# Kernel tuning notes

Measured on AMD Instinct MI355X. Metric: run time of the kernel, lower is better.

## Reference

```python
import jax, jax.numpy as jnp
import numpy as np

D = 256   # state.D, per-node vector width
B = 16    # batch
L = 8     # depth layers (hidden), all < t_budget
N = 128   # nodes per depth layer
LAMBDA_ASYNC = 0.08
LAMBDA_TAU = 0.12
BOOST_SCALE = 1.0


def setup_inputs() -> dict:
    key = jax.random.key(0)
    ks = jax.random.split(key, 6)
    X = jax.random.normal(ks[0], (B, D), jnp.float32)
    # per-node weight matrices, scaled so tanh stays in linear-ish regime
    W = jax.random.normal(ks[1], (L, N, D, D), jnp.float32) / np.sqrt(D).astype(np.float32)
    bias = jax.random.normal(ks[2], (L, N, D), jnp.float32) * 0.01
    S = jax.random.normal(ks[3], (L, N, D), jnp.float32) / np.sqrt(D).astype(np.float32)
    rho = jax.random.uniform(ks[4], (L, N), jnp.float32, minval=0.2, maxval=0.6)
    boost = jax.random.normal(ks[5], (L, N), jnp.float32) * 0.01  # residue.decode(node_id)
    return {"X": X, "W": W, "bias": bias, "S": S, "rho": rho, "boost": boost, "t_budget": 15}


def reference(X, W, bias, S, rho, boost, t_budget):
    # Messages routed at depth d are consumed at depth d+1 -> decay = exp(-lambda_async * 1)
    decay = jnp.exp(jnp.float32(-LAMBDA_ASYNC))
    tb = jnp.float32(t_budget)

    def step(carry, layer):
        V_in, has_input = carry            # V_in: (B, D) aggregated inbox, shared under dense routing
        Wl, bl, Sl, rl, gl, depth = layer  # (N,D,D), (N,D), (N,D), (N,), (N,), scalar
        # anytime threshold tau(t) = 0.5 * exp(lambda_tau * (t - t_budget))
        tau = 0.5 * jnp.exp(LAMBDA_TAU * (depth - tb))
        # s_dot.mean(): mean over batch of <V_in, S_n>, per node -> (N,)
        s_dot = jnp.einsum('bd,nd->n', V_in, Sl) / jnp.float32(B)
        rho_active = rl + s_dot + gl * BOOST_SCALE
        fired = (rho_active >= tau) & has_input                      # (N,) thresholded firing
        # V_weighted = apply_W_batch(V_in) + bias, per node
        V_w = jnp.einsum('bd,nde->nbe', V_in, Wl) + bl[:, None, :]   # (N, B, D)
        V_out = jnp.tanh(V_w)                                        # pointwise primitive
        fmask = fired.astype(V_out.dtype)
        cnt = jnp.maximum(fmask.sum(), jnp.float32(1.0))
        # inbox aggregation at next depth: decayed mean over fired contributors
        V_next = decay * jnp.einsum('n,nbe->be', fmask, V_out) / cnt
        return (V_next, fmask.sum() > 0), (V_out, fired)

    depths = jnp.arange(1, L + 1, dtype=jnp.float32)
    (_, _), (V_all, fired_all) = jax.lax.scan(
        step, (X, jnp.array(True)), (W, bias, S, rho, boost, depths))
    # output = mean over fired output-layer (last depth) nodes
    last_V, last_f = V_all[-1], fired_all[-1]
    fm = last_f.astype(last_V.dtype)
    out = jnp.einsum('n,nbe->be', fm, last_V) / jnp.maximum(fm.sum(), jnp.float32(1.0))
    return out
```

## Files before the change

### kernel.cpp

```cpp
#include <hip/hip_runtime.h>
#include <math.h>

#define D 256
#define B 16
#define L 8
#define N 128

static constexpr float LAMBDA_ASYNC = 0.08f;
static constexpr float LAMBDA_TAU   = 0.12f;


#define OFF_COLSUM 4096
#define OFF_META   4352
#define OFF_FIRED  4368
#define OFF_SLAB   4496

__global__ __launch_bounds__(512) void layer_kernel(
    const float* __restrict__ Wl,
    const float* __restrict__ biasl,
    const float* __restrict__ Sl,
    const float* __restrict__ rhol,
    const float* __restrict__ boostl,
    const int*  __restrict__ tb,
    const float* __restrict__ vin_src,
    const float* __restrict__ X,
    const float* __restrict__ colsum,
    const float* __restrict__ meta_prev,
    float* __restrict__ slab,
    float* __restrict__ fired_cur,
    float depth, int is_first)
{
    __shared__ float vin[D * 16];
    __shared__ float red[4 * 64 * 33];
    __shared__ float sh[8];

    const int t    = threadIdx.x;
    const int w    = t >> 6;
    const int lane = t & 63;
    const int n    = blockIdx.x >> 1;
    const int h    = blockIdx.x & 1;
    const int e0   = h * 128;

    float part = 0.0f;
    if (is_first) {
        if (t < 256) {
            #pragma unroll
            for (int b = 0; b < 16; ++b) vin[t * 16 + b] = X[b * 256 + t];
        }
        __syncthreads();
        if (t < 256) {
            const float4 a0 = *(const float4*)&vin[t * 16 + 0];
            const float4 a1 = *(const float4*)&vin[t * 16 + 4];
            const float4 a2 = *(const float4*)&vin[t * 16 + 8];
            const float4 a3 = *(const float4*)&vin[t * 16 + 12];
            const float cs = a0.x + a0.y + a0.z + a0.w + a1.x + a1.y + a1.z + a1.w
                           + a2.x + a2.y + a2.z + a2.w + a3.x + a3.y + a3.z + a3.w;
            part = cs * Sl[n * D + t];
        }
    } else {
        if (t < 256) part = colsum[t] * Sl[n * D + t];
    }
    #pragma unroll
    for (int o = 32; o > 0; o >>= 1) part += __shfl_down(part, o);
    if (lane == 0) sh[w] = part;
    __syncthreads();

    {
        const bool has_input = is_first ? true : (meta_prev[0] > 0.0f);
        const float sdot = (sh[0] + sh[1] + sh[2] + sh[3]) * (1.0f / 16.0f);
        const float tau  = 0.5f * expf(LAMBDA_TAU * (depth - (float)tb[0]));
        const bool fired = (rhol[n] + sdot + boostl[n] >= tau) && has_input;
        if (h == 0 && t == 0) fired_cur[n] = fired ? 1.0f : 0.0f;
        if (!fired) return;
    }

    if (!is_first) {
        const float4* s4 = (const float4*)vin_src;
        ((float4*)vin)[t * 2 + 0] = s4[t * 2 + 0];
        ((float4*)vin)[t * 2 + 1] = s4[t * 2 + 1];
        __syncthreads();
    }

    const float* wp = Wl + (size_t)n * D * D + (e0 + lane * 2);
    const int dbase = w * 32;

    float accA[16], accB[16];
    #pragma unroll
    for (int b = 0; b < 16; ++b) { accA[b] = 0.0f; accB[b] = 0.0f; }

    #pragma unroll
    for (int j = 0; j < 32; j += 4) {
        float2 wv[4];
        #pragma unroll
        for (int i = 0; i < 4; ++i)
            wv[i] = *(const float2*)(wp + (size_t)(dbase + j + i) * 256);
        #pragma unroll
        for (int i = 0; i < 4; ++i) {
            const float* vr = &vin[(dbase + j + i) * 16];
            const float4 v0 = *(const float4*)(vr + 0);
            const float4 v1 = *(const float4*)(vr + 4);
            const float4 v2 = *(const float4*)(vr + 8);
            const float4 v3 = *(const float4*)(vr + 12);
            const float wx = wv[i].x, wy = wv[i].y;
            accA[ 0] = fmaf(wx, v0.x, accA[ 0]); accB[ 0] = fmaf(wy, v0.x, accB[ 0]);
            accA[ 1] = fmaf(wx, v0.y, accA[ 1]); accB[ 1] = fmaf(wy, v0.y, accB[ 1]);
            accA[ 2] = fmaf(wx, v0.z, accA[ 2]); accB[ 2] = fmaf(wy, v0.z, accB[ 2]);
            accA[ 3] = fmaf(wx, v0.w, accA[ 3]); accB[ 3] = fmaf(wy, v0.w, accB[ 3]);
            accA[ 4] = fmaf(wx, v1.x, accA[ 4]); accB[ 4] = fmaf(wy, v1.x, accB[ 4]);
            accA[ 5] = fmaf(wx, v1.y, accA[ 5]); accB[ 5] = fmaf(wy, v1.y, accB[ 5]);
            accA[ 6] = fmaf(wx, v1.z, accA[ 6]); accB[ 6] = fmaf(wy, v1.z, accB[ 6]);
            accA[ 7] = fmaf(wx, v1.w, accA[ 7]); accB[ 7] = fmaf(wy, v1.w, accB[ 7]);
            accA[ 8] = fmaf(wx, v2.x, accA[ 8]); accB[ 8] = fmaf(wy, v2.x, accB[ 8]);
            accA[ 9] = fmaf(wx, v2.y, accA[ 9]); accB[ 9] = fmaf(wy, v2.y, accB[ 9]);
            accA[10] = fmaf(wx, v2.z, accA[10]); accB[10] = fmaf(wy, v2.z, accB[10]);
            accA[11] = fmaf(wx, v2.w, accA[11]); accB[11] = fmaf(wy, v2.w, accB[11]);
            accA[12] = fmaf(wx, v3.x, accA[12]); accB[12] = fmaf(wy, v3.x, accB[12]);
            accA[13] = fmaf(wx, v3.y, accA[13]); accB[13] = fmaf(wy, v3.y, accB[13]);
            accA[14] = fmaf(wx, v3.z, accA[14]); accB[14] = fmaf(wy, v3.z, accB[14]);
            accA[15] = fmaf(wx, v3.w, accA[15]); accB[15] = fmaf(wy, v3.w, accB[15]);
        }
    }

    {
        float* rr = &red[((w & 3) * 64 + lane) * 33];
        if (w >= 4) {
            #pragma unroll
            for (int b = 0; b < 16; ++b) { rr[b] = accA[b]; rr[16 + b] = accB[b]; }
        }
        __syncthreads();
        if (w < 4) {
            #pragma unroll
            for (int b = 0; b < 16; ++b) { rr[b] += accA[b]; rr[16 + b] += accB[b]; }
        }
        __syncthreads();
    }

    {
        const int e_loc = t >> 2;
        const int b0    = (t & 3) * 4;
        const int lane2 = e_loc >> 1;
        const int sub   = e_loc & 1;
        const int o0    = sub * 16 + b0;
        const float bv  = biasl[n * D + e0 + e_loc];
        float4 o4;
        o4.x = tanhf(red[(0*64+lane2)*33 + o0+0] + red[(1*64+lane2)*33 + o0+0]
                   + red[(2*64+lane2)*33 + o0+0] + red[(3*64+lane2)*33 + o0+0] + bv);
        o4.y = tanhf(red[(0*64+lane2)*33 + o0+1] + red[(1*64+lane2)*33 + o0+1]
                   + red[(2*64+lane2)*33 + o0+1] + red[(3*64+lane2)*33 + o0+1] + bv);
        o4.z = tanhf(red[(0*64+lane2)*33 + o0+2] + red[(1*64+lane2)*33 + o0+2]
                   + red[(2*64+lane2)*33 + o0+2] + red[(3*64+lane2)*33 + o0+2] + bv);
        o4.w = tanhf(red[(0*64+lane2)*33 + o0+3] + red[(1*64+lane2)*33 + o0+3]
                   + red[(2*64+lane2)*33 + o0+3] + red[(3*64+lane2)*33 + o0+3] + bv);
        *(float4*)(slab + (size_t)n * 4096 + (size_t)(e0 + e_loc) * 16 + b0) = o4;
    }
}

template<bool IS_FINAL>
__global__ __launch_bounds__(256) void reduce_kernel(
    const float* __restrict__ slab, const float* __restrict__ fired_l,
    float* __restrict__ acct, float* __restrict__ colsum,
    float* __restrict__ meta, float* __restrict__ out)
{
    __shared__ float part[256];
    __shared__ float shcnt;
    const int t    = threadIdx.x;
    const int cell = blockIdx.x * 64 + (t & 63);
    const int n0   = (t >> 6) * 32;

    float s = 0.0f;
    #pragma unroll 8
    for (int k = 0; k < 32; ++k)
        s = fmaf(fired_l[n0 + k], slab[(size_t)(n0 + k) * 4096 + cell], s);
    part[t] = s;

    if (t < 64) {
        float c = fired_l[t] + fired_l[t + 64];
        #pragma unroll
        for (int o = 32; o > 0; o >>= 1) c += __shfl_down(c, o);
        if (t == 0) shcnt = c;
    }
    __syncthreads();

    if (t < 64) {
        const float cnt = shcnt;
        const int c = blockIdx.x * 64 + t;
        const float tot = part[t] + part[64 + t] + part[128 + t] + part[192 + t];
        if (IS_FINAL) {
            out[(c & 15) * 256 + (c >> 4)] = tot / fmaxf(cnt, 1.0f);
        } else {
            const float scale = expf(-LAMBDA_ASYNC) / fmaxf(cnt, 1.0f);
            const float v = tot * scale;
            acct[c] = v;
            float cs = v;
            cs += __shfl_down(cs, 8);
            cs += __shfl_down(cs, 4);
            cs += __shfl_down(cs, 2);
            cs += __shfl_down(cs, 1);
            if ((t & 15) == 0) colsum[c >> 4] = cs;
            if (blockIdx.x == 0 && t == 0) meta[0] = cnt;
        }
    }
}

extern "C" void kernel_launch(void* const* d_in, const int* in_sizes, int n_in,
                              void* d_out, int out_size, void* d_ws, size_t ws_size,
                              hipStream_t stream)
{
    const float* X     = (const float*)d_in[0];
    const float* W     = (const float*)d_in[1];
    const float* bias  = (const float*)d_in[2];
    const float* S     = (const float*)d_in[3];
    const float* rho   = (const float*)d_in[4];
    const float* boost = (const float*)d_in[5];
    const int*   tb    = (const int*)d_in[6];
    float* out = (float*)d_out;
    float* ws  = (float*)d_ws;

    float* acct   = ws;
    float* colsum = ws + OFF_COLSUM;
    float* meta   = ws + OFF_META;
    float* fired  = ws + OFF_FIRED;
    float* slab   = ws + OFF_SLAB;

    for (int l = 0; l < L; ++l) {
        layer_kernel<<<dim3(256), dim3(512), 0, stream>>>(
            W + (size_t)l * N * D * D,
            bias + (size_t)l * N * D,
            S + (size_t)l * N * D,
            rho + (size_t)l * N,
            boost + (size_t)l * N,
            tb,
            acct, X, colsum,
            (l == 0) ? (const float*)nullptr : meta,
            slab, fired,
            (float)(l + 1), (l == 0) ? 1 : 0);
        if (l < L - 1) {
            reduce_kernel<false><<<dim3(64), dim3(256), 0, stream>>>(
                slab, fired, acct, colsum, meta, out);
        } else {
            reduce_kernel<true><<<dim3(64), dim3(256), 0, stream>>>(
                slab, fired, acct, colsum, meta, out);
        }
    }
}
```

Before: 117.3 us.

## Split layer GEMV into quarter-width blocks using readlane broadcast of inputs

The layer kernel now launches four blocks per node, each covering 64 output columns, so the grid doubles to 512 blocks. Each lane loads one weight per row and broadcasts the 16 batch inputs across the wave with readlane, which replaces the float4 LDS reads and halves the accumulators. The 8-wave reduction becomes a single shared-memory pass with padded rows. A separate transpose kernel prepares the transposed X and its column sums before layer 0, so the first layer no longer carries a special path. The trade-off is narrower, less coalesced weight loads, per-element readlane overhead, and one extra kernel launch.

```diff
diff --git a/kernel.cpp b/kernel.cpp
--- a/kernel.cpp
+++ b/kernel.cpp
@@ -14,6 +14,20 @@
 #define OFF_META   4352
 #define OFF_FIRED  4368
 #define OFF_SLAB   4496
+
+__global__ __launch_bounds__(256) void transpose_kernel(
+    const float* __restrict__ X, float* __restrict__ xt,
+    float* __restrict__ colsum) {
+    const int d = threadIdx.x;
+    float cs = 0.0f;
+    #pragma unroll
+    for (int b = 0; b < B; ++b) {
+        const float v = X[b * D + d];
+        xt[d * 16 + b] = v;
+        cs += v;
+    }
+    colsum[d] = cs;
+}
 
 __global__ __launch_bounds__(512) void layer_kernel(
     const float* __restrict__ Wl,
@@ -23,7 +37,6 @@
     const float* __restrict__ boostl,
     const int*  __restrict__ tb,
     const float* __restrict__ vin_src,
-    const float* __restrict__ X,
     const float* __restrict__ colsum,
     const float* __restrict__ meta_prev,
     float* __restrict__ slab,
@@ -31,127 +44,78 @@
     float depth, int is_first)
 {
     __shared__ float vin[D * 16];
-    __shared__ float red[4 * 64 * 33];
+    __shared__ float red[8 * 64 * 17];
     __shared__ float sh[8];
 
     const int t    = threadIdx.x;
     const int w    = t >> 6;
     const int lane = t & 63;
-    const int n    = blockIdx.x >> 1;
-    const int h    = blockIdx.x & 1;
-    const int e0   = h * 128;
+    const int n    = blockIdx.x >> 2;
+    const int e0   = (blockIdx.x & 3) * 64;
 
     float part = 0.0f;
-    if (is_first) {
-        if (t < 256) {
-            #pragma unroll
-            for (int b = 0; b < 16; ++b) vin[t * 16 + b] = X[b * 256 + t];
-        }
-        __syncthreads();
-        if (t < 256) {
-            const float4 a0 = *(const float4*)&vin[t * 16 + 0];
-            const float4 a1 = *(const float4*)&vin[t * 16 + 4];
-            const float4 a2 = *(const float4*)&vin[t * 16 + 8];
-            const float4 a3 = *(const float4*)&vin[t * 16 + 12];
-            const float cs = a0.x + a0.y + a0.z + a0.w + a1.x + a1.y + a1.z + a1.w
-                           + a2.x + a2.y + a2.z + a2.w + a3.x + a3.y + a3.z + a3.w;
-            part = cs * Sl[n * D + t];
-        }
-    } else {
-        if (t < 256) part = colsum[t] * Sl[n * D + t];
-    }
+    if (t < 256) part = colsum[t] * Sl[n * D + t];
     #pragma unroll
     for (int o = 32; o > 0; o >>= 1) part += __shfl_down(part, o);
     if (lane == 0) sh[w] = part;
     __syncthreads();
-
     {
         const bool has_input = is_first ? true : (meta_prev[0] > 0.0f);
         const float sdot = (sh[0] + sh[1] + sh[2] + sh[3]) * (1.0f / 16.0f);
         const float tau  = 0.5f * expf(LAMBDA_TAU * (depth - (float)tb[0]));
         const bool fired = (rhol[n] + sdot + boostl[n] >= tau) && has_input;
-        if (h == 0 && t == 0) fired_cur[n] = fired ? 1.0f : 0.0f;
+        if ((blockIdx.x & 3) == 0 && t == 0) fired_cur[n] = fired ? 1.0f : 0.0f;
         if (!fired) return;
     }
 
-    if (!is_first) {
+    {
         const float4* s4 = (const float4*)vin_src;
         ((float4*)vin)[t * 2 + 0] = s4[t * 2 + 0];
         ((float4*)vin)[t * 2 + 1] = s4[t * 2 + 1];
-        __syncthreads();
-    }
-
-    const float* wp = Wl + (size_t)n * D * D + (e0 + lane * 2);
+    }
+    __syncthreads();
+
     const int dbase = w * 32;
-
-    float accA[16], accB[16];
+    const float* wp = Wl + ((size_t)n * D + (size_t)dbase) * D + (e0 + lane);
+
+    float acc[16];
     #pragma unroll
-    for (int b = 0; b < 16; ++b) { accA[b] = 0.0f; accB[b] = 0.0f; }
-
-    #pragma unroll
-    for (int j = 0; j < 32; j += 4) {
-        float2 wv[4];
-        #pragma unroll
-        for (int i = 0; i < 4; ++i)
-            wv[i] = *(const float2*)(wp + (size_t)(dbase + j + i) * 256);
-        #pragma unroll
-        for (int i = 0; i < 4; ++i) {
-            const float* vr = &vin[(dbase + j + i) * 16];
-            const float4 v0 = *(const float4*)(vr + 0);
-            const float4 v1 = *(const float4*)(vr + 4);
-            const float4 v2 = *(const float4*)(vr + 8);
-            const float4 v3 = *(const float4*)(vr + 12);
-            const float wx = wv[i].x, wy = wv[i].y;
-            accA[ 0] = fmaf(wx, v0.x, accA[ 0]); accB[ 0] = fmaf(wy, v0.x, accB[ 0]);
-            accA[ 1] = fmaf(wx, v0.y, accA[ 1]); accB[ 1] = fmaf(wy, v0.y, accB[ 1]);
-            accA[ 2] = fmaf(wx, v0.z, accA[ 2]); accB[ 2] = fmaf(wy, v0.z, accB[ 2]);
-            accA[ 3] = fmaf(wx, v0.w, accA[ 3]); accB[ 3] = fmaf(wy, v0.w, accB[ 3]);
-            accA[ 4] = fmaf(wx, v1.x, accA[ 4]); accB[ 4] = fmaf(wy, v1.x, accB[ 4]);
-            accA[ 5] = fmaf(wx, v1.y, accA[ 5]); accB[ 5] = fmaf(wy, v1.y, accB[ 5]);
-            accA[ 6] = fmaf(wx, v1.z, accA[ 6]); accB[ 6] = fmaf(wy, v1.z, accB[ 6]);
-            accA[ 7] = fmaf(wx, v1.w, accA[ 7]); accB[ 7] = fmaf(wy, v1.w, accB[ 7]);
-            accA[ 8] = fmaf(wx, v2.x, accA[ 8]); accB[ 8] = fmaf(wy, v2.x, accB[ 8]);
-            accA[ 9] = fmaf(wx, v2.y, accA[ 9]); accB[ 9] = fmaf(wy, v2.y, accB[ 9]);
-            accA[10] = fmaf(wx, v2.z, accA[10]); accB[10] = fmaf(wy, v2.z, accB[10]);
-            accA[11] = fmaf(wx, v2.w, accA[11]); accB[11] = fmaf(wy, v2.w, accB[11]);
-            accA[12] = fmaf(wx, v3.x, accA[12]); accB[12] = fmaf(wy, v3.x, accB[12]);
-            accA[13] = fmaf(wx, v3.y, accA[13]); accB[13] = fmaf(wy, v3.y, accB[13]);
-            accA[14] = fmaf(wx, v3.z, accA[14]); accB[14] = fmaf(wy, v3.z, accB[14]);
-            accA[15] = fmaf(wx, v3.w, accA[15]); accB[15] = fmaf(wy, v3.w, accB[15]);
-        }
-    }
-
-    {
-        float* rr = &red[((w & 3) * 64 + lane) * 33];
-        if (w >= 4) {
-            #pragma unroll
-            for (int b = 0; b < 16; ++b) { rr[b] = accA[b]; rr[16 + b] = accB[b]; }
-        }
-        __syncthreads();
-        if (w < 4) {
-            #pragma unroll
-            for (int b = 0; b < 16; ++b) { rr[b] += accA[b]; rr[16 + b] += accB[b]; }
-        }
-        __syncthreads();
-    }
-
-    {
-        const int e_loc = t >> 2;
-        const int b0    = (t & 3) * 4;
-        const int lane2 = e_loc >> 1;
-        const int sub   = e_loc & 1;
-        const int o0    = sub * 16 + b0;
-        const float bv  = biasl[n * D + e0 + e_loc];
-        float4 o4;
-        o4.x = tanhf(red[(0*64+lane2)*33 + o0+0] + red[(1*64+lane2)*33 + o0+0]
-                   + red[(2*64+lane2)*33 + o0+0] + red[(3*64+lane2)*33 + o0+0] + bv);
-        o4.y = tanhf(red[(0*64+lane2)*33 + o0+1] + red[(1*64+lane2)*33 + o0+1]
-                   + red[(2*64+lane2)*33 + o0+1] + red[(3*64+lane2)*33 + o0+1] + bv);
-        o4.z = tanhf(red[(0*64+lane2)*33 + o0+2] + red[(1*64+lane2)*33 + o0+2]
-                   + red[(2*64+lane2)*33 + o0+2] + red[(3*64+lane2)*33 + o0+2] + bv);
-        o4.w = tanhf(red[(0*64+lane2)*33 + o0+3] + red[(1*64+lane2)*33 + o0+3]
-                   + red[(2*64+lane2)*33 + o0+3] + red[(3*64+lane2)*33 + o0+3] + bv);
-        *(float4*)(slab + (size_t)n * 4096 + (size_t)(e0 + e_loc) * 16 + b0) = o4;
+    for (int b = 0; b < 16; ++b) acc[b] = 0.0f;
+
+    #pragma unroll 8
+    for (int r = 0; r < 32; ++r) {
+        const float wj = wp[(size_t)r * D];
+        const float vv = vin[(dbase + r) * 16 + (lane & 15)];
+        #pragma unroll
+        for (int b = 0; b < 16; ++b) {
+            const float rb = __uint_as_float(
+                __builtin_amdgcn_readlane(__float_as_uint(vv), b));
+            acc[b] = fmaf(wj, rb, acc[b]);
+        }
+    }
+
+    {
+        float* rr = &red[(w * 64 + lane) * 17];
+        #pragma unroll
+        for (int b = 0; b < 16; ++b) rr[b] = acc[b];
+    }
+    __syncthreads();
+
+    {
+        const int e_loc = t & 63;
+        const int p     = t >> 6;
+        float s0 = 0.0f, s1 = 0.0f;
+        #pragma unroll
+        for (int w2 = 0; w2 < 8; ++w2) {
+            const float* rr = &red[(w2 * 64 + e_loc) * 17];
+            s0 += rr[2 * p];
+            s1 += rr[2 * p + 1];
+        }
+        const float bv = biasl[n * D + e0 + e_loc];
+        float2 o;
+        o.x = tanhf(s0 + bv);
+        o.y = tanhf(s1 + bv);
+        *(float2*)(slab + (size_t)n * 4096 + (size_t)(e0 + e_loc) * 16 + 2 * p) = o;
     }
 }
 
@@ -222,15 +186,17 @@
     float* fired  = ws + OFF_FIRED;
     float* slab   = ws + OFF_SLAB;
 
+    transpose_kernel<<<dim3(1), dim3(256), 0, stream>>>(X, acct, colsum);
+
     for (int l = 0; l < L; ++l) {
-        layer_kernel<<<dim3(256), dim3(512), 0, stream>>>(
+        layer_kernel<<<dim3(512), dim3(512), 0, stream>>>(
             W + (size_t)l * N * D * D,
             bias + (size_t)l * N * D,
             S + (size_t)l * N * D,
             rho + (size_t)l * N,
             boost + (size_t)l * N,
             tb,
-            acct, X, colsum,
+            acct, colsum,
             (l == 0) ? (const float*)nullptr : meta,
             slab, fired,
             (float)(l + 1), (l == 0) ? 1 : 0);
```

Result: slower. 132.0 us (+12.5%).

## Split per-node matvec across D halves and move bias+tanh into reduce

Applied to the files above, without the earlier changes.

Each node's matvec is now split over both the input dimension and the output dimension, using four 256-thread blocks per node instead of two 512-thread blocks. Partial sums are written to a doubled slab, and the reduce kernel adds the two halves, applies bias and tanh, then does the masked mean. A small transpose prepass computes the first-layer inbox and its column sums, so the layer kernel no longer needs a first-layer special case. The aim is more, smaller blocks that spread weight streaming and hide latency better. In exchange, slab traffic doubles, tanh runs in the lower-parallelism reduce kernel, and the path depends on having a larger workspace.

```diff
diff --git a/kernel.cpp b/kernel.cpp
--- a/kernel.cpp
+++ b/kernel.cpp
@@ -15,73 +15,66 @@
 #define OFF_FIRED  4368
 #define OFF_SLAB   4496
 
-__global__ __launch_bounds__(512) void layer_kernel(
-    const float* __restrict__ Wl,
-    const float* __restrict__ biasl,
-    const float* __restrict__ Sl,
-    const float* __restrict__ rhol,
-    const float* __restrict__ boostl,
+__global__ __launch_bounds__(256) void transpose_kernel(
+    const float* __restrict__ X, float* __restrict__ xt,
+    float* __restrict__ colsum) {
+    const int d = threadIdx.x;
+    float cs = 0.0f;
+    #pragma unroll
+    for (int b = 0; b < B; ++b) {
+        const float v = X[b * D + d];
+        xt[d * 16 + b] = v;
+        cs += v;
+    }
+    colsum[d] = cs;
+}
+
+__global__ __launch_bounds__(256) void layer_split(
+    const float* __restrict__ Wl, const float* __restrict__ Sl,
+    const float* __restrict__ rhol, const float* __restrict__ boostl,
     const int*  __restrict__ tb,
     const float* __restrict__ vin_src,
-    const float* __restrict__ X,
     const float* __restrict__ colsum,
     const float* __restrict__ meta_prev,
     float* __restrict__ slab,
     float* __restrict__ fired_cur,
     float depth, int is_first)
 {
-    __shared__ float vin[D * 16];
-    __shared__ float red[4 * 64 * 33];
-    __shared__ float sh[8];
+    __shared__ float vin[128 * 16];
+    __shared__ float red[2 * 64 * 33];
+    __shared__ float sh[4];
 
     const int t    = threadIdx.x;
     const int w    = t >> 6;
     const int lane = t & 63;
-    const int n    = blockIdx.x >> 1;
-    const int h    = blockIdx.x & 1;
-    const int e0   = h * 128;
-
-    float part = 0.0f;
-    if (is_first) {
-        if (t < 256) {
-            #pragma unroll
-            for (int b = 0; b < 16; ++b) vin[t * 16 + b] = X[b * 256 + t];
-        }
-        __syncthreads();
-        if (t < 256) {
-            const float4 a0 = *(const float4*)&vin[t * 16 + 0];
-            const float4 a1 = *(const float4*)&vin[t * 16 + 4];
-            const float4 a2 = *(const float4*)&vin[t * 16 + 8];
-            const float4 a3 = *(const float4*)&vin[t * 16 + 12];
-            const float cs = a0.x + a0.y + a0.z + a0.w + a1.x + a1.y + a1.z + a1.w
-                           + a2.x + a2.y + a2.z + a2.w + a3.x + a3.y + a3.z + a3.w;
-            part = cs * Sl[n * D + t];
-        }
-    } else {
-        if (t < 256) part = colsum[t] * Sl[n * D + t];
-    }
+    const int n    = blockIdx.x >> 2;
+    const int dh   = (blockIdx.x >> 1) & 1;
+    const int eh   = blockIdx.x & 1;
+    const int e0   = eh * 128;
+    const int d0   = dh * 128;
+
+    float part = colsum[t] * Sl[n * D + t];
     #pragma unroll
     for (int o = 32; o > 0; o >>= 1) part += __shfl_down(part, o);
     if (lane == 0) sh[w] = part;
     __syncthreads();
-
     {
         const bool has_input = is_first ? true : (meta_prev[0] > 0.0f);
         const float sdot = (sh[0] + sh[1] + sh[2] + sh[3]) * (1.0f / 16.0f);
         const float tau  = 0.5f * expf(LAMBDA_TAU * (depth - (float)tb[0]));
         const bool fired = (rhol[n] + sdot + boostl[n] >= tau) && has_input;
-        if (h == 0 && t == 0) fired_cur[n] = fired ? 1.0f : 0.0f;
+        if ((blockIdx.x & 3) == 0 && t == 0) fired_cur[n] = fired ? 1.0f : 0.0f;
         if (!fired) return;
     }
 
-    if (!is_first) {
-        const float4* s4 = (const float4*)vin_src;
+    {
+        const float4* s4 = (const float4*)vin_src + (size_t)d0 * 4;
         ((float4*)vin)[t * 2 + 0] = s4[t * 2 + 0];
         ((float4*)vin)[t * 2 + 1] = s4[t * 2 + 1];
-        __syncthreads();
-    }
-
-    const float* wp = Wl + (size_t)n * D * D + (e0 + lane * 2);
+    }
+    __syncthreads();
+
+    const float* wp = Wl + ((size_t)n * D + (size_t)(d0 + w * 32)) * D + (e0 + lane * 2);
     const int dbase = w * 32;
 
     float accA[16], accB[16];
@@ -93,7 +86,7 @@
         float2 wv[4];
         #pragma unroll
         for (int i = 0; i < 4; ++i)
-            wv[i] = *(const float2*)(wp + (size_t)(dbase + j + i) * 256);
+            wv[i] = *(const float2*)(wp + (size_t)(j + i) * 256);
         #pragma unroll
         for (int i = 0; i < 4; ++i) {
             const float* vr = &vin[(dbase + j + i) * 16];
@@ -122,13 +115,13 @@
     }
 
     {
-        float* rr = &red[((w & 3) * 64 + lane) * 33];
-        if (w >= 4) {
+        float* rr = &red[((w & 1) * 64 + lane) * 33];
+        if (w >= 2) {
             #pragma unroll
             for (int b = 0; b < 16; ++b) { rr[b] = accA[b]; rr[16 + b] = accB[b]; }
         }
         __syncthreads();
-        if (w < 4) {
+        if (w < 2) {
             #pragma unroll
             for (int b = 0; b < 16; ++b) { rr[b] += accA[b]; rr[16 + b] += accB[b]; }
         }
@@ -136,28 +129,27 @@
     }
 
     {
-        const int e_loc = t >> 2;
-        const int b0    = (t & 3) * 4;
+        const int e_loc = t & 127;
+        const int b0    = (t >> 7) * 8;
         const int lane2 = e_loc >> 1;
         const int sub   = e_loc & 1;
         const int o0    = sub * 16 + b0;
-        const float bv  = biasl[n * D + e0 + e_loc];
-        float4 o4;
-        o4.x = tanhf(red[(0*64+lane2)*33 + o0+0] + red[(1*64+lane2)*33 + o0+0]
-                   + red[(2*64+lane2)*33 + o0+0] + red[(3*64+lane2)*33 + o0+0] + bv);
-        o4.y = tanhf(red[(0*64+lane2)*33 + o0+1] + red[(1*64+lane2)*33 + o0+1]
-                   + red[(2*64+lane2)*33 + o0+1] + red[(3*64+lane2)*33 + o0+1] + bv);
-        o4.z = tanhf(red[(0*64+lane2)*33 + o0+2] + red[(1*64+lane2)*33 + o0+2]
-                   + red[(2*64+lane2)*33 + o0+2] + red[(3*64+lane2)*33 + o0+2] + bv);
-        o4.w = tanhf(red[(0*64+lane2)*33 + o0+3] + red[(1*64+lane2)*33 + o0+3]
-                   + red[(2*64+lane2)*33 + o0+3] + red[(3*64+lane2)*33 + o0+3] + bv);
-        *(float4*)(slab + (size_t)n * 4096 + (size_t)(e0 + e_loc) * 16 + b0) = o4;
+        float s[8];
+        #pragma unroll
+        for (int j = 0; j < 8; ++j)
+            s[j] = red[(0 * 64 + lane2) * 33 + o0 + j]
+                 + red[(1 * 64 + lane2) * 33 + o0 + j];
+        float* dst = slab + ((size_t)(n * 2 + dh)) * 4096
+                   + (size_t)(e0 + e_loc) * 16 + b0;
+        *(float4*)(dst + 0) = make_float4(s[0], s[1], s[2], s[3]);
+        *(float4*)(dst + 4) = make_float4(s[4], s[5], s[6], s[7]);
     }
 }
 
 template<bool IS_FINAL>
-__global__ __launch_bounds__(256) void reduce_kernel(
-    const float* __restrict__ slab, const float* __restrict__ fired_l,
+__global__ __launch_bounds__(256) void reduce_split(
+    const float* __restrict__ slab, const float* __restrict__ biasl,
+    const float* __restrict__ fired_l,
     float* __restrict__ acct, float* __restrict__ colsum,
     float* __restrict__ meta, float* __restrict__ out)
 {
@@ -166,11 +158,16 @@
     const int t    = threadIdx.x;
     const int cell = blockIdx.x * 64 + (t & 63);
     const int n0   = (t >> 6) * 32;
+    const int e    = cell >> 4;
 
     float s = 0.0f;
     #pragma unroll 8
-    for (int k = 0; k < 32; ++k)
-        s = fmaf(fired_l[n0 + k], slab[(size_t)(n0 + k) * 4096 + cell], s);
+    for (int k = 0; k < 32; ++k) {
+        const int n = n0 + k;
+        const float p = slab[((size_t)(n * 2 + 0)) * 4096 + cell]
+                      + slab[((size_t)(n * 2 + 1)) * 4096 + cell];
+        s = fmaf(fired_l[n], tanhf(p + biasl[n * D + e]), s);
+    }
     part[t] = s;
 
     if (t < 64) {
@@ -202,6 +199,163 @@
     }
 }
 
+__global__ __launch_bounds__(512) void layer_full(
+    const float* __restrict__ Wl, const float* __restrict__ biasl,
+    const float* __restrict__ Sl, const float* __restrict__ rhol,
+    const float* __restrict__ boostl, const int* __restrict__ tb,
+    const float* __restrict__ vin_src, const float* __restrict__ colsum,
+    const float* __restrict__ meta_prev,
+    float* __restrict__ slab, float* __restrict__ fired_cur,
+    float depth, int is_first)
+{
+    __shared__ float vin[D * 16];
+    __shared__ float red[4 * 64 * 33];
+    __shared__ float sh[8];
+
+    const int t    = threadIdx.x;
+    const int w    = t >> 6;
+    const int lane = t & 63;
+    const int n    = blockIdx.x >> 1;
+    const int e0   = (blockIdx.x & 1) * 128;
+
+    float part = 0.0f;
+    if (t < 256) part = colsum[t] * Sl[n * D + t];
+    #pragma unroll
+    for (int o = 32; o > 0; o >>= 1) part += __shfl_down(part, o);
+    if (lane == 0) sh[w] = part;
+    __syncthreads();
+    {
+        const bool has_input = is_first ? true : (meta_prev[0] > 0.0f);
+        const float sdot = (sh[0] + sh[1] + sh[2] + sh[3]) * (1.0f / 16.0f);
+        const float tau  = 0.5f * expf(LAMBDA_TAU * (depth - (float)tb[0]));
+        const bool fired = (rhol[n] + sdot + boostl[n] >= tau) && has_input;
+        if ((blockIdx.x & 1) == 0 && t == 0) fired_cur[n] = fired ? 1.0f : 0.0f;
+        if (!fired) return;
+    }
+    {
+        const float4* s4 = (const float4*)vin_src;
+        ((float4*)vin)[t * 2 + 0] = s4[t * 2 + 0];
+        ((float4*)vin)[t * 2 + 1] = s4[t * 2 + 1];
+        __syncthreads();
+    }
+
+    const float* wp = Wl + (size_t)n * D * D + (e0 + lane * 2);
+    const int dbase = w * 32;
+    float accA[16], accB[16];
+    #pragma unroll
+    for (int b = 0; b < 16; ++b) { accA[b] = 0.0f; accB[b] = 0.0f; }
+    #pragma unroll
+    for (int j = 0; j < 32; j += 4) {
+        float2 wv[4];
+        #pragma unroll
+        for (int i = 0; i < 4; ++i)
+            wv[i] = *(const float2*)(wp + (size_t)(dbase + j + i) * 256);
+        #pragma unroll
+        for (int i = 0; i < 4; ++i) {
+            const float* vr = &vin[(dbase + j + i) * 16];
+            const float4 v0 = *(const float4*)(vr + 0);
+            const float4 v1 = *(const float4*)(vr + 4);
+            const float4 v2 = *(const float4*)(vr + 8);
+            const float4 v3 = *(const float4*)(vr + 12);
+            const float wx = wv[i].x, wy = wv[i].y;
+            accA[ 0] = fmaf(wx, v0.x, accA[ 0]); accB[ 0] = fmaf(wy, v0.x, accB[ 0]);
+            accA[ 1] = fmaf(wx, v0.y, accA[ 1]); accB[ 1] = fmaf(wy, v0.y, accB[ 1]);
+            accA[ 2] = fmaf(wx, v0.z, accA[ 2]); accB[ 2] = fmaf(wy, v0.z, accB[ 2]);
+            accA[ 3] = fmaf(wx, v0.w, accA[ 3]); accB[ 3] = fmaf(wy, v0.w, accB[ 3]);
+            accA[ 4] = fmaf(wx, v1.x, accA[ 4]); accB[ 4] = fmaf(wy, v1.x, accB[ 4]);
+            accA[ 5] = fmaf(wx, v1.y, accA[ 5]); accB[ 5] = fmaf(wy, v1.y, accB[ 5]);
+            accA[ 6] = fmaf(wx, v1.z, accA[ 6]); accB[ 6] = fmaf(wy, v1.z, accB[ 6]);
+            accA[ 7] = fmaf(wx, v1.w, accA[ 7]); accB[ 7] = fmaf(wy, v1.w, accB[ 7]);
+            accA[ 8] = fmaf(wx, v2.x, accA[ 8]); accB[ 8] = fmaf(wy, v2.x, accB[ 8]);
+            accA[ 9] = fmaf(wx, v2.y, accA[ 9]); accB[ 9] = fmaf(wy, v2.y, accB[ 9]);
+            accA[10] = fmaf(wx, v2.z, accA[10]); accB[10] = fmaf(wy, v2.z, accB[10]);
+            accA[11] = fmaf(wx, v2.w, accA[11]); accB[11] = fmaf(wy, v2.w, accB[11]);
+            accA[12] = fmaf(wx, v3.x, accA[12]); accB[12] = fmaf(wy, v3.x, accB[12]);
+            accA[13] = fmaf(wx, v3.y, accA[13]); accB[13] = fmaf(wy, v3.y, accB[13]);
+            accA[14] = fmaf(wx, v3.z, accA[14]); accB[14] = fmaf(wy, v3.z, accB[14]);
+            accA[15] = fmaf(wx, v3.w, accA[15]); accB[15] = fmaf(wy, v3.w, accB[15]);
+        }
+    }
+    {
+        float* rr = &red[((w & 3) * 64 + lane) * 33];
+        if (w >= 4) {
+            #pragma unroll
+            for (int b = 0; b < 16; ++b) { rr[b] = accA[b]; rr[16 + b] = accB[b]; }
+        }
+        __syncthreads();
+        if (w < 4) {
+            #pragma unroll
+            for (int b = 0; b < 16; ++b) { rr[b] += accA[b]; rr[16 + b] += accB[b]; }
+        }
+        __syncthreads();
+    }
+    {
+        const int e_loc = t >> 2;
+        const int b0    = (t & 3) * 4;
+        const int lane2 = e_loc >> 1;
+        const int sub   = e_loc & 1;
+        const int o0    = sub * 16 + b0;
+        const float bv  = biasl[n * D + e0 + e_loc];
+        float4 o4;
+        o4.x = tanhf(red[(0*64+lane2)*33 + o0+0] + red[(1*64+lane2)*33 + o0+0]
+                   + red[(2*64+lane2)*33 + o0+0] + red[(3*64+lane2)*33 + o0+0] + bv);
+        o4.y = tanhf(red[(0*64+lane2)*33 + o0+1] + red[(1*64+lane2)*33 + o0+1]
+                   + red[(2*64+lane2)*33 + o0+1] + red[(3*64+lane2)*33 + o0+1] + bv);
+        o4.z = tanhf(red[(0*64+lane2)*33 + o0+2] + red[(1*64+lane2)*33 + o0+2]
+                   + red[(2*64+lane2)*33 + o0+2] + red[(3*64+lane2)*33 + o0+2] + bv);
+        o4.w = tanhf(red[(0*64+lane2)*33 + o0+3] + red[(1*64+lane2)*33 + o0+3]
+                   + red[(2*64+lane2)*33 + o0+3] + red[(3*64+lane2)*33 + o0+3] + bv);
+        *(float4*)(slab + (size_t)n * 4096 + (size_t)(e0 + e_loc) * 16 + b0) = o4;
+    }
+}
+
+template<bool IS_FINAL>
+__global__ __launch_bounds__(256) void reduce_full(
+    const float* __restrict__ slab, const float* __restrict__ fired_l,
+    float* __restrict__ acct, float* __restrict__ colsum,
+    float* __restrict__ meta, float* __restrict__ out)
+{
+    __shared__ float part[256];
+    __shared__ float shcnt;
+    const int t    = threadIdx.x;
+    const int cell = blockIdx.x * 64 + (t & 63);
+    const int n0   = (t >> 6) * 32;
+
+    float s = 0.0f;
+    #pragma unroll 8
+    for (int k = 0; k < 32; ++k)
+        s = fmaf(fired_l[n0 + k], slab[(size_t)(n0 + k) * 4096 + cell], s);
+    part[t] = s;
+
+    if (t < 64) {
+        float c = fired_l[t] + fired_l[t + 64];
+        #pragma unroll
+        for (int o = 32; o > 0; o >>= 1) c += __shfl_down(c, o);
+        if (t == 0) shcnt = c;
+    }
+    __syncthreads();
+
+    if (t < 64) {
+        const float cnt = shcnt;
+        const int c = blockIdx.x * 64 + t;
+        const float tot = part[t] + part[64 + t] + part[128 + t] + part[192 + t];
+        if (IS_FINAL) {
+            out[(c & 15) * 256 + (c >> 4)] = tot / fmaxf(cnt, 1.0f);
+        } else {
+            const float scale = expf(-LAMBDA_ASYNC) / fmaxf(cnt, 1.0f);
+            const float v = tot * scale;
+            acct[c] = v;
+            float cs = v;
+            cs += __shfl_down(cs, 8);
+            cs += __shfl_down(cs, 4);
+            cs += __shfl_down(cs, 2);
+            cs += __shfl_down(cs, 1);
+            if ((t & 15) == 0) colsum[c >> 4] = cs;
+            if (blockIdx.x == 0 && t == 0) meta[0] = cnt;
+        }
+    }
+}
+
 extern "C" void kernel_launch(void* const* d_in, const int* in_sizes, int n_in,
                               void* d_out, int out_size, void* d_ws, size_t ws_size,
                               hipStream_t stream)
@@ -222,24 +376,38 @@
     float* fired  = ws + OFF_FIRED;
     float* slab   = ws + OFF_SLAB;
 
+    const bool split = ws_size >= (size_t)(OFF_SLAB + N * 2 * 4096) * sizeof(float);
+
+    transpose_kernel<<<dim3(1), dim3(256), 0, stream>>>(X, acct, colsum);
+
     for (int l = 0; l < L; ++l) {
-        layer_kernel<<<dim3(256), dim3(512), 0, stream>>>(
-            W + (size_t)l * N * D * D,
-            bias + (size_t)l * N * D,
-            S + (size_t)l * N * D,
-            rho + (size_t)l * N,
-            boost + (size_t)l * N,
-            tb,
-            acct, X, colsum,
-            (l == 0) ? (const float*)nullptr : meta,
-            slab, fired,
-            (float)(l + 1), (l == 0) ? 1 : 0);
-        if (l < L - 1) {
-            reduce_kernel<false><<<dim3(64), dim3(256), 0, stream>>>(
-                slab, fired, acct, colsum, meta, out);
+        const float* Wl = W + (size_t)l * N * D * D;
+        const float* bl = bias + (size_t)l * N * D;
+        const float* Sl = S + (size_t)l * N * D;
+        const float* rl = rho + (size_t)l * N;
+        const float* gl = boost + (size_t)l * N;
+        const float* mp = (l == 0) ? (const float*)nullptr : meta;
+        const float dep = (float)(l + 1);
+        const int first = (l == 0) ? 1 : 0;
+
+        if (split) {
+            layer_split<<<dim3(N * 4), dim3(256), 0, stream>>>(
+                Wl, Sl, rl, gl, tb, acct, colsum, mp, slab, fired, dep, first);
+            if (l < L - 1)
+                reduce_split<false><<<dim3(64), dim3(256), 0, stream>>>(
+                    slab, bl, fired, acct, colsum, meta, out);
+            else
+                reduce_split<true><<<dim3(64), dim3(256), 0, stream>>>(
+                    slab, bl, fired, acct, colsum, meta, out);
         } else {
-            reduce_kernel<true><<<dim3(64), dim3(256), 0, stream>>>(
-                slab, fired, acct, colsum, meta, out);
-        }
-    }
-}
+            layer_full<<<dim3(N * 2), dim3(512), 0, stream>>>(
+                Wl, bl, Sl, rl, gl, tb, acct, colsum, mp, slab, fired, dep, first);
+            if (l < L - 1)
+                reduce_full<false><<<dim3(64), dim3(256), 0, stream>>>(
+                    slab, fired, acct, colsum, meta, out);
+            else
+                reduce_full<true><<<dim3(64), dim3(256), 0, stream>>>(
+                    slab, fired, acct, colsum, meta, out);
+        }
+    }
+}
```

After: 204.1 us. 1.74x slower.
